# Kernel optimization log

Measured on AMD Instinct MI355X. Metric: run time of the kernel, lower is better.

The kernel has to match this reference:

```python
import jax, jax.numpy as jnp
import numpy as np
import math

B, S = 1, 2048
HID = 2048
H = 16
Q_LORA = 1536
KV_LORA = 512
ROPE_D = 64
NOPE_D = 128
V_D = 128
Q_HD = NOPE_D + ROPE_D  # 192
THETA = 10000.0
EPS = 1e-6


def rmsnorm(x, w):
    xf = x.astype(jnp.float32)
    n = xf * jax.lax.rsqrt(jnp.mean(xf * xf, axis=-1, keepdims=True) + EPS)
    return n.astype(x.dtype) * w


def rotate_half(x):
    d = x.shape[-1] // 2
    return jnp.concatenate([-x[..., d:], x[..., :d]], axis=-1)


def setup_inputs() -> dict:
    key = jax.random.key(0)
    ks = jax.random.split(key, 8)
    std = 0.02
    x = jax.random.normal(ks[0], (B, S, HID), dtype=jnp.float32)
    position = jnp.broadcast_to(jnp.arange(S, dtype=jnp.int32), (B, S))
    mask = jnp.broadcast_to(jnp.tril(jnp.ones((S, S), dtype=jnp.int32)), (B, S, S))
    Wq_down = jax.random.normal(ks[1], (HID, Q_LORA), dtype=jnp.float32) * std
    q_norm_w = jnp.ones((Q_LORA,), dtype=jnp.float32)
    Wq_up = jax.random.normal(ks[2], (Q_LORA, H * Q_HD), dtype=jnp.float32) * std
    Wkv_down = jax.random.normal(ks[3], (HID, KV_LORA + ROPE_D), dtype=jnp.float32) * std
    kv_norm_w = jnp.ones((KV_LORA,), dtype=jnp.float32)
    Wkv_up = jax.random.normal(ks[4], (KV_LORA, H * (NOPE_D + V_D)), dtype=jnp.float32) * std
    Wout = jax.random.normal(ks[5], (HID, HID), dtype=jnp.float32) * std
    return {"x": x, "position": position, "mask": mask,
            "Wq_down": Wq_down, "q_norm_w": q_norm_w, "Wq_up": Wq_up,
            "Wkv_down": Wkv_down, "kv_norm_w": kv_norm_w, "Wkv_up": Wkv_up,
            "Wout": Wout}


def reference(x, position, mask, Wq_down, q_norm_w, Wq_up, Wkv_down, kv_norm_w, Wkv_up, Wout):
    b, s, _ = x.shape
    # --- Q path: low-rank down -> RMSNorm -> up ---
    q = rmsnorm(x @ Wq_down, q_norm_w) @ Wq_up            # [B,S,H*Q_HD]
    q = q.reshape(b, s, H, Q_HD).transpose(0, 2, 1, 3)    # [B,H,S,Q_HD]
    q_nope, q_rope = q[..., :NOPE_D], q[..., NOPE_D:]
    # --- KV path ---
    c = x @ Wkv_down                                       # [B,S,KV_LORA+ROPE_D]
    c_kv, k_rope = c[..., :KV_LORA], c[..., KV_LORA:]
    kv = rmsnorm(c_kv, kv_norm_w) @ Wkv_up                 # [B,S,H*(NOPE_D+V_D)]
    kv = kv.reshape(b, s, H, NOPE_D + V_D).transpose(0, 2, 1, 3)
    k_nope, v_state = kv[..., :NOPE_D], kv[..., NOPE_D:]
    k_rope = k_rope[:, None]                               # [B,1,S,ROPE_D]
    # --- RoPE (decoupled, on rope dims only) ---
    inv_freq = 1.0 / (THETA ** (jnp.arange(0, ROPE_D, 2, dtype=jnp.float32) / ROPE_D))
    t = jnp.arange(s, dtype=jnp.float32)
    freqs = jnp.outer(t, inv_freq)                         # [S,ROPE_D/2]
    emb = jnp.concatenate([freqs, freqs], axis=-1)         # [S,ROPE_D]
    cos = jnp.cos(emb)[position][:, None]                  # [B,1,S,ROPE_D]
    sin = jnp.sin(emb)[position][:, None]
    q_rope = q_rope * cos + rotate_half(q_rope) * sin      # [B,H,S,ROPE_D]
    k_rope = k_rope * cos + rotate_half(k_rope) * sin      # [B,1,S,ROPE_D]
    k_rope = jnp.broadcast_to(k_rope, (b, H, s, ROPE_D))
    q_state = jnp.concatenate([q_nope, q_rope], axis=-1)   # [B,H,S,Q_HD]
    k_state = jnp.concatenate([k_nope, k_rope], axis=-1)   # [B,H,S,Q_HD]
    # --- attention (note: original scales by sqrt(v_head_dim)) ---
    scores = jnp.einsum('bhqd,bhkd->bhqk', q_state, k_state) / math.sqrt(V_D)
    scores = jnp.where(mask[:, None] == 0, -jnp.inf, scores)
    att_w = jax.nn.softmax(scores, axis=-1)
    att = jnp.einsum('bhqk,bhkd->bhqd', att_w, v_state)    # [B,H,S,V_D]
    att = att.transpose(0, 2, 1, 3).reshape(b, s, H * V_D) # [B,S,HID]
    return att @ Wout
```

## Files before the change

kernel.cpp:

```cpp
#include <hip/hip_runtime.h>
#include <hip/hip_bf16.h>
#include <math.h>

typedef __bf16 bf16_t;
typedef __bf16 bf16x4 __attribute__((ext_vector_type(4)));
typedef __bf16 bf16x8 __attribute__((ext_vector_type(8)));
typedef float f32x4 __attribute__((ext_vector_type(4)));

#define LOG2E 1.4426950408889634f

typedef const __attribute__((address_space(1))) void* as1cv;
typedef __attribute__((address_space(3))) void* as3v;

__device__ __forceinline__ void gload16(const bf16_t* g, bf16_t* l) {
  __builtin_amdgcn_global_load_lds((as1cv)g, (as3v)l, 16, 0, 0);
}

__global__ __launch_bounds__(256)
void prep_k(const float* __restrict__ x, const float* __restrict__ Wqd,
            const float* __restrict__ Wkvd, const float* __restrict__ Wqu,
            const float* __restrict__ Wkvu, const float* __restrict__ Wout,
            bf16_t* __restrict__ xb, bf16_t* __restrict__ WdT,
            bf16_t* __restrict__ WquT, bf16_t* __restrict__ WkvuT,
            bf16_t* __restrict__ WoutT) {
  __shared__ float t[32][33];
  const int tid = threadIdx.x;
  int bid = blockIdx.x;
  if (bid < 4096) {
    int i = (bid * 256 + tid) * 4;
    float4 v = *(const float4*)(x + i);
    bf16x4 o;
    o[0] = (bf16_t)v.x; o[1] = (bf16_t)v.y; o[2] = (bf16_t)v.z; o[3] = (bf16_t)v.w;
    *(bf16x4*)(xb + i) = o;
    return;
  }
  bid -= 4096;
  const float* in; bf16_t* out; int C, R, bx, by;
  if (bid < 3072)       { in = Wqd;  out = WdT;           R = 2048; C = 1536; bx = bid % 48;  by = bid / 48; }
  else if (bid < 4224)  { int b = bid - 3072;  in = Wkvd; out = WdT + 3145728; R = 2048; C = 576;  bx = b % 18;  by = b / 18; }
  else if (bid < 8832)  { int b = bid - 4224;  in = Wqu;  out = WquT;  R = 1536; C = 3072; bx = b % 96;  by = b / 96; }
  else if (bid < 10880) { int b = bid - 8832;  in = Wkvu; out = WkvuT; R = 512;  C = 4096; bx = b % 128; by = b / 128; }
  else                  { int b = bid - 10880; in = Wout; out = WoutT; R = 2048; C = 2048; bx = b % 64;  by = b / 64; }
  const int c0 = bx * 32, r0 = by * 32;
  const int tx = tid & 31, ty = tid >> 5;
#pragma unroll
  for (int i = 0; i < 32; i += 8)
    t[ty + i][tx] = in[(size_t)(r0 + ty + i) * C + c0 + tx];
  __syncthreads();
#pragma unroll
  for (int i = 0; i < 32; i += 8)
    out[(size_t)(c0 + ty + i) * R + r0 + tx] = (bf16_t)t[tx][ty + i];
}


__device__ __forceinline__ void stage8(const bf16_t* __restrict__ A,
                                       const bf16_t* __restrict__ Bt,
                                       int K, int N, int m0, int n0, int k0,
                                       bf16_t* As, bf16_t* Bs,
                                       int wave, int srow, int scol) {
#pragma unroll
  for (int i = 0; i < 2; ++i) {
    int r0 = (wave * 2 + i) * 8;
    gload16(A + (size_t)(m0 + r0 + srow) * K + k0 + scol, As + r0 * 64);
    int br = n0 + r0 + srow;
    if (br >= N) br = N - 1;
    gload16(Bt + (size_t)br * K + k0 + scol, Bs + r0 * 64);
  }
}

__device__ __forceinline__ void compute8(const bf16_t* As, const bf16_t* Bs,
                                         f32x4 (&acc)[2][4],
                                         int lane, int wr, int wc) {
  const int lm = lane & 15;
  const int sw = lm & 7;
#pragma unroll
  for (int ks = 0; ks < 2; ++ks) {
    const int ck = ((lane >> 4) + ks * 4) ^ sw;
    bf16x8 af[2], bfr[4];
#pragma unroll
    for (int i = 0; i < 2; ++i)
      af[i] = *(const bf16x8*)(As + (wr + i * 16 + lm) * 64 + ck * 8);
#pragma unroll
    for (int i = 0; i < 4; ++i)
      bfr[i] = *(const bf16x8*)(Bs + (wc + i * 16 + lm) * 64 + ck * 8);
#pragma unroll
    for (int mi = 0; mi < 2; ++mi)
#pragma unroll
      for (int ni = 0; ni < 4; ++ni)
        acc[mi][ni] = __builtin_amdgcn_mfma_f32_16x16x32_bf16(
            af[mi], bfr[ni], acc[mi][ni], 0, 0, 0);
  }
}

#define VMCNT(n) asm volatile("s_waitcnt vmcnt(" #n ")" ::: "memory")

__device__ __forceinline__ void gemm128_dbuf8(const bf16_t* __restrict__ A,
                                              const bf16_t* __restrict__ Bt,
                                              int K, int N, int m0, int n0,
                                              bf16_t* lds, f32x4 (&acc)[2][4],
                                              int wave, int lane) {
  const int srow = lane >> 3;
  const int scol = ((lane & 7) ^ srow) * 8;
  const int wr = (wave >> 1) * 32, wc = (wave & 1) * 64;
  bf16_t* A0 = lds;
  bf16_t* B0 = lds + 8192;
  bf16_t* A1 = lds + 16384;
  bf16_t* B1 = lds + 24576;
  const int nk = K >> 6;
  stage8(A, Bt, K, N, m0, n0, 0, A0, B0, wave, srow, scol);
  stage8(A, Bt, K, N, m0, n0, 64, A1, B1, wave, srow, scol);
  VMCNT(4);
  __builtin_amdgcn_s_barrier();
#pragma unroll 1
  for (int t = 0; t < nk; t += 2) {
    compute8(A0, B0, acc, lane, wr, wc);
    __builtin_amdgcn_s_barrier();
    if (t + 2 < nk) {
      stage8(A, Bt, K, N, m0, n0, (t + 2) << 6, A0, B0, wave, srow, scol);
      VMCNT(4);
    } else {
      VMCNT(0);
    }
    __builtin_amdgcn_s_barrier();
    compute8(A1, B1, acc, lane, wr, wc);
    if (t + 3 <= nk) {
      __builtin_amdgcn_s_barrier();
      if (t + 3 < nk) {
        stage8(A, Bt, K, N, m0, n0, (t + 3) << 6, A1, B1, wave, srow, scol);
        VMCNT(4);
      } else {
        VMCNT(0);
      }
      __builtin_amdgcn_s_barrier();
    }
  }
}

__global__ __launch_bounds__(512)
void gemm_dn8(const bf16_t* __restrict__ A, const bf16_t* __restrict__ Bt,
              bf16_t* __restrict__ C, int M, int N, int K) {
  __shared__ __align__(16) bf16_t lds[32768];
  const int tid = threadIdx.x;
  const int wave = tid >> 6, lane = tid & 63;
  const int m0 = blockIdx.y * 128, n0 = blockIdx.x * 128;
  const int wr = (wave >> 1) * 32, wc = (wave & 1) * 64;
  f32x4 acc[2][4] = {};
  gemm128_dbuf8(A, Bt, K, N, m0, n0, lds, acc, wave, lane);
  const int lm = lane & 15, lr = (lane >> 4) * 4;
#pragma unroll
  for (int mi = 0; mi < 2; ++mi)
#pragma unroll
    for (int ni = 0; ni < 4; ++ni) {
      int col = n0 + wc + ni * 16 + lm;
      if (col < N) {
#pragma unroll
        for (int i = 0; i < 4; ++i) {
          int row = m0 + wr + mi * 16 + lr + i;
          C[(size_t)row * N + col] = (bf16_t)acc[mi][ni][i];
        }
      }
    }
}

__global__ __launch_bounds__(512)
void gemm_outf8(const bf16_t* __restrict__ A, const bf16_t* __restrict__ Bt,
                float* __restrict__ C, int M, int N, int K) {
  __shared__ __align__(16) bf16_t lds[32768];
  const int tid = threadIdx.x;
  const int wave = tid >> 6, lane = tid & 63;
  const int m0 = blockIdx.y * 128, n0 = blockIdx.x * 128;
  const int wr = (wave >> 1) * 32, wc = (wave & 1) * 64;
  f32x4 acc[2][4] = {};
  gemm128_dbuf8(A, Bt, K, N, m0, n0, lds, acc, wave, lane);
  const int lm = lane & 15, lr = (lane >> 4) * 4;
#pragma unroll
  for (int mi = 0; mi < 2; ++mi)
#pragma unroll
    for (int ni = 0; ni < 4; ++ni) {
      int col = n0 + wc + ni * 16 + lm;
#pragma unroll
      for (int i = 0; i < 4; ++i) {
        int row = m0 + wr + mi * 16 + lr + i;
        C[(size_t)row * N + col] = acc[mi][ni][i];
      }
    }
}

__global__ __launch_bounds__(512)
void gemm_qkvup8(const bf16_t* __restrict__ qdn, const bf16_t* __restrict__ WquT,
                 const bf16_t* __restrict__ ckvn, const bf16_t* __restrict__ WkvuT,
                 const int* __restrict__ pos, bf16_t* __restrict__ qs,
                 bf16_t* __restrict__ ks, bf16_t* __restrict__ vt) {
  __shared__ __align__(16) bf16_t lds[32768];
  const int tid = threadIdx.x;
  const int wave = tid >> 6, lane = tid & 63;
  const int m0 = blockIdx.y * 128;
  const int wr = (wave >> 1) * 32, wc = (wave & 1) * 64;
  const int lm = lane & 15, lr = (lane >> 4) * 4;
  f32x4 acc[2][4] = {};
  if (blockIdx.x < 24) {
    const int n0 = blockIdx.x * 128;
    gemm128_dbuf8(qdn, WquT, 1536, 3072, m0, n0, lds, acc, wave, lane);
    const bool rope = (((n0 + wc) / 64) % 3) == 2;
    if (rope) {
#pragma unroll
      for (int mi = 0; mi < 2; ++mi)
#pragma unroll
        for (int i = 0; i < 4; ++i) {
          int row = m0 + wr + mi * 16 + lr + i;
          float p = (float)pos[row];
#pragma unroll
          for (int nl = 0; nl < 2; ++nl) {
            int fi = nl * 16 + lm;
            float ang = p * exp2f(-(float)fi * 0.41524101186092030f);
            float sn, cs;
            sincosf(ang, &sn, &cs);
            float v0 = acc[mi][nl][i], v1 = acc[mi][nl + 2][i];
            int c = n0 + wc + nl * 16 + lm;
            int h = c / 192, d = c - h * 192;
            bf16_t* base = qs + ((size_t)h * 2048 + row) * 192;
            base[d]      = (bf16_t)(v0 * cs - v1 * sn);
            base[d + 32] = (bf16_t)(v1 * cs + v0 * sn);
          }
        }
    } else {
#pragma unroll
      for (int mi = 0; mi < 2; ++mi)
#pragma unroll
        for (int ni = 0; ni < 4; ++ni) {
          int c = n0 + wc + ni * 16 + lm;
          int h = c / 192, d = c - h * 192;
#pragma unroll
          for (int i = 0; i < 4; ++i) {
            int row = m0 + wr + mi * 16 + lr + i;
            qs[((size_t)h * 2048 + row) * 192 + d] = (bf16_t)acc[mi][ni][i];
          }
        }
    }
  } else {
    const int n0 = (blockIdx.x - 24) * 128;
    gemm128_dbuf8(ckvn, WkvuT, 512, 4096, m0, n0, lds, acc, wave, lane);
#pragma unroll
    for (int mi = 0; mi < 2; ++mi)
#pragma unroll
      for (int ni = 0; ni < 4; ++ni) {
        int c = n0 + wc + ni * 16 + lm;
        int h = c >> 8, j = c & 255;
#pragma unroll
        for (int i = 0; i < 4; ++i) {
          int row = m0 + wr + mi * 16 + lr + i;
          bf16_t v = (bf16_t)acc[mi][ni][i];
          if (j < 128)
            ks[((size_t)h * 2048 + row) * 192 + j] = v;
          else
            vt[((size_t)h * 128 + (j - 128)) * 2048 + row] = v;
        }
      }
  }
}

__global__ __launch_bounds__(256)
void normrope_k(const bf16_t* __restrict__ Cd, const float* __restrict__ qnw,
                const float* __restrict__ kvnw, const int* __restrict__ pos,
                bf16_t* __restrict__ qdn, bf16_t* __restrict__ ckvn,
                bf16_t* __restrict__ ks) {
  __shared__ float red[4];
  const int bid = blockIdx.x, tid = threadIdx.x;
  if (bid < 4096) {
    const bf16_t* xr;
    const float* W;
    bf16_t* yr;
    int C;
    if (bid < 2048) {
      xr = Cd + (size_t)bid * 2112; W = qnw; yr = qdn + (size_t)bid * 1536; C = 1536;
    } else {
      int r = bid - 2048;
      xr = Cd + (size_t)r * 2112 + 1536; W = kvnw; yr = ckvn + (size_t)r * 512; C = 512;
    }
    int nch = C >> 3;
    bool act = tid < nch;
    float xv[8];
    float ss = 0.f;
    if (act) {
      bf16x8 v = *(const bf16x8*)(xr + tid * 8);
#pragma unroll
      for (int i = 0; i < 8; ++i) { xv[i] = (float)v[i]; ss += xv[i] * xv[i]; }
    }
#pragma unroll
    for (int off = 1; off < 64; off <<= 1) ss += __shfl_xor(ss, off, 64);
    if ((tid & 63) == 0) red[tid >> 6] = ss;
    __syncthreads();
    float tot = red[0] + red[1] + red[2] + red[3];
    float rs = rsqrtf(tot / (float)C + 1e-6f);
    if (act) {
      bf16x8 o;
#pragma unroll
      for (int i = 0; i < 8; ++i) {
        bf16_t nb = (bf16_t)(xv[i] * rs);
        o[i] = (bf16_t)((float)nb * W[tid * 8 + i]);
      }
      *(bf16x8*)(yr + tid * 8) = o;
    }
  } else {
    int s = bid - 4096, d = tid;
    if (d < 64) {
      float v = (float)Cd[(size_t)s * 2112 + 2048 + d];
      int fi = d & 31;
      float p = (float)pos[s];
      float ang = p * exp2f(-(float)fi * 0.415241011860920295f);
      float sn = sinf(ang), co = cosf(ang);
      float other = (float)Cd[(size_t)s * 2112 + 2048 + (d < 32 ? d + 32 : d - 32)];
      v = (d < 32) ? v * co - other * sn : v * co + other * sn;
      bf16_t bv = (bf16_t)v;
#pragma unroll
      for (int h = 0; h < 16; ++h)
        ks[((size_t)h * 2048 + s) * 192 + 128 + d] = bv;
    }
  }
}

__global__ __launch_bounds__(256)
void attn3_k(const bf16_t* __restrict__ Q, const bf16_t* __restrict__ Kst,
             const bf16_t* __restrict__ Vt, bf16_t* __restrict__ O,
             float* __restrict__ pbuf) {
  __shared__ __align__(16) bf16_t Ks[64 * 192];
  __shared__ __align__(16) bf16_t Vs[144 * 64];
  __shared__ __align__(16) bf16_t Ps[4][16 * 72];
  const int bid = blockIdx.x + (blockIdx.y << 8);
  const int lo = bid & 255;
  const int h = lo >> 4;
  const int jj = lo & 15;
  int t, kbeg, kend, sp = 0, pidx = 0;
  bool direct = false;
  if (bid < 256)      { t = 16 + jj; kbeg = 0;  kend = 16;    sp = 0; pidx = jj; }
  else if (bid < 512) { t = jj;      kbeg = 0;  kend = t + 1; direct = true; }
  else                { t = 31 - jj; kbeg = 16; kend = t + 1; sp = 1; pidx = 15 - jj; }
  const int q0 = t * 64;
  const int tid = threadIdx.x, wave = tid >> 6, lane = tid & 63;
  const int lm = lane & 15, lg = lane >> 4;
  const bf16_t* Qh = Q + (size_t)h * 2048 * 192;
  const bf16_t* Kh = Kst + (size_t)h * 2048 * 192;
  const bf16_t* Vh = Vt + (size_t)h * 128 * 2048;
  const float sc = 0.08838834764831845f * LOG2E;

  bf16x8 aq[6];
#pragma unroll
  for (int tt = 0; tt < 6; ++tt)
    aq[tt] = *(const bf16x8*)(Qh + (size_t)(q0 + wave * 16 + lm) * 192 + tt * 32 + lg * 8);

#pragma unroll
  for (int w = 0; w < 4; ++w) {
    int idx = w * 256 + tid;
    Vs[128 * 64 + idx] = (bf16_t)(idx < 64 ? 1.0f : 0.0f);
  }

  int kr[6], kc8[6], vr[4], vc8[4];
#pragma unroll
  for (int w = 0; w < 6; ++w) {
    int s = (wave * 6 + w) * 64 + lane;
    kr[w] = s / 24;
    kc8[w] = ((s % 24) ^ (kr[w] & 7)) * 8;
  }
#pragma unroll
  for (int w = 0; w < 4; ++w) {
    int s = (wave * 4 + w) * 64 + lane;
    vr[w] = s >> 3;
    vc8[w] = ((s & 7) ^ (vr[w] & 7)) * 8;
  }

  bf16x8 kstg[6], vstg[4];
  const int kb0 = kbeg * 64;
#pragma unroll
  for (int w = 0; w < 6; ++w)
    kstg[w] = *(const bf16x8*)(Kh + (size_t)(kb0 + kr[w]) * 192 + kc8[w]);
#pragma unroll
  for (int w = 0; w < 4; ++w)
    vstg[w] = *(const bf16x8*)(Vh + (size_t)vr[w] * 2048 + kb0 + vc8[w]);

  f32x4 o[9] = {};

  for (int kt = kbeg; kt < kend; ++kt) {
    const int k0 = kt * 64;
    if (kt != kbeg) __syncthreads();
#pragma unroll
    for (int w = 0; w < 6; ++w)
      *(bf16x8*)(Ks + ((wave * 6 + w) * 64 + lane) * 8) = kstg[w];
#pragma unroll
    for (int w = 0; w < 4; ++w)
      *(bf16x8*)(Vs + ((wave * 4 + w) * 64 + lane) * 8) = vstg[w];
    __syncthreads();

    if (kt + 1 < kend) {
      const int k1 = k0 + 64;
#pragma unroll
      for (int w = 0; w < 6; ++w)
        kstg[w] = *(const bf16x8*)(Kh + (size_t)(k1 + kr[w]) * 192 + kc8[w]);
#pragma unroll
      for (int w = 0; w < 4; ++w)
        vstg[w] = *(const bf16x8*)(Vh + (size_t)vr[w] * 2048 + k1 + vc8[w]);
    }

    f32x4 sa[4] = {};
    __builtin_amdgcn_s_setprio(1);
#pragma unroll
    for (int ct = 0; ct < 4; ++ct) {
#pragma unroll
      for (int tt = 0; tt < 6; ++tt) {
        int cc = (tt * 4 + lg) ^ (lm & 7);
        bf16x8 bk = *(const bf16x8*)(Ks + (ct * 16 + lm) * 192 + cc * 8);
        sa[ct] = __builtin_amdgcn_mfma_f32_16x16x32_bf16(aq[tt], bk, sa[ct], 0, 0, 0);
      }
    }
    __builtin_amdgcn_s_setprio(0);

    bf16_t* Pw = Ps[wave];
    const bool diag = (kt == t);
#pragma unroll
    for (int i = 0; i < 4; ++i) {
      const int row = q0 + wave * 16 + lg * 4 + i;
#pragma unroll
      for (int ct = 0; ct < 4; ++ct) {
        float p = exp2f(sa[ct][i] * sc);
        if (diag && (k0 + ct * 16 + lm > row)) p = 0.f;
        Pw[(lg * 4 + i) * 72 + ct * 16 + lm] = (bf16_t)p;
      }
    }
    __builtin_amdgcn_s_waitcnt(0xC07F);

    __builtin_amdgcn_s_setprio(1);
#pragma unroll
    for (int ks2 = 0; ks2 < 2; ++ks2) {
      bf16x8 ap = *(const bf16x8*)(Pw + lm * 72 + ks2 * 32 + lg * 8);
#pragma unroll
      for (int nt = 0; nt < 9; ++nt) {
        int rowv = nt * 16 + lm;
        int cc = (ks2 * 4 + lg) ^ (lm & 7);
        bf16x8 bv = *(const bf16x8*)(Vs + rowv * 64 + cc * 8);
        o[nt] = __builtin_amdgcn_mfma_f32_16x16x32_bf16(ap, bv, o[nt], 0, 0, 0);
      }
    }
    __builtin_amdgcn_s_setprio(0);
  }

  if (direct) {
#pragma unroll
    for (int i = 0; i < 4; ++i) {
      float l = __shfl(o[8][i], (lane & 48), 64);
      float inv = 1.f / l;
      int row = q0 + wave * 16 + lg * 4 + i;
#pragma unroll
      for (int nt = 0; nt < 8; ++nt)
        O[(size_t)row * 2048 + h * 128 + nt * 16 + lm] = (bf16_t)(o[nt][i] * inv);
    }
  } else {
    float* P = pbuf + ((size_t)(h * 16 + pidx) * 2 + sp) * 8448;
#pragma unroll
    for (int i = 0; i < 4; ++i) {
      int r = wave * 16 + lg * 4 + i;
#pragma unroll
      for (int nt = 0; nt < 8; ++nt)
        P[r * 132 + nt * 16 + lm] = o[nt][i];
      if (lm == 0) P[r * 132 + 128] = o[8][i];
    }
  }
}

__global__ __launch_bounds__(256)
void combine_k(const float* __restrict__ pbuf, bf16_t* __restrict__ O) {
  const int b = blockIdx.x, tid = threadIdx.x;
  const int h = b >> 4, pidx = b & 15;
  const int r = tid >> 2, c0 = (tid & 3) * 32;
  const float* p0 = pbuf + ((size_t)(h * 16 + pidx) * 2) * 8448 + r * 132;
  const float* p1 = p0 + 8448;
  const float inv = 1.f / (p0[128] + p1[128]);
  const int row = (16 + pidx) * 64 + r;
  bf16_t* dst = O + (size_t)row * 2048 + h * 128 + c0;
#pragma unroll
  for (int i = 0; i < 32; i += 4) {
    float4 a = *(const float4*)(p0 + c0 + i);
    float4 c = *(const float4*)(p1 + c0 + i);
    bf16x4 v;
    v[0] = (bf16_t)((a.x + c.x) * inv);
    v[1] = (bf16_t)((a.y + c.y) * inv);
    v[2] = (bf16_t)((a.z + c.z) * inv);
    v[3] = (bf16_t)((a.w + c.w) * inv);
    *(bf16x4*)(dst + i) = v;
  }
}

extern "C" void kernel_launch(void* const* d_in, const int* in_sizes, int n_in,
                              void* d_out, int out_size, void* d_ws, size_t ws_size,
                              hipStream_t stream) {
  const float* x    = (const float*)d_in[0];
  const int*   pos  = (const int*)d_in[1];
  const float* Wqd  = (const float*)d_in[3];
  const float* qnw  = (const float*)d_in[4];
  const float* Wqu  = (const float*)d_in[5];
  const float* Wkvd = (const float*)d_in[6];
  const float* kvnw = (const float*)d_in[7];
  const float* Wkvu = (const float*)d_in[8];
  const float* Wout = (const float*)d_in[9];
  float* out = (float*)d_out;

  bf16_t* arena = (bf16_t*)d_ws;
  bf16_t* xb    = arena;
  bf16_t* attb  = arena;
  bf16_t* WdT   = arena + 4194304;
  bf16_t* qdn   = arena + 4194304;
  bf16_t* WquT  = arena + 8519680;
  bf16_t* WkvuT = arena + 13238272;
  float*  pbuf  = (float*)(arena + 4194304);
  bf16_t* WoutT = arena + 15335424;
  bf16_t* Cdown = arena + 19529728;
  bf16_t* vt    = arena + 19529728;
  bf16_t* qs    = arena + 23855104;
  bf16_t* ks    = arena + 30146560;
  bf16_t* ckvn  = arena + 36438016;

  prep_k<<<dim3(19072), 256, 0, stream>>>(x, Wqd, Wkvd, Wqu, Wkvu, Wout,
                                          xb, WdT, WquT, WkvuT, WoutT);

  gemm_dn8<<<dim3(17, 16), 512, 0, stream>>>(xb, WdT, Cdown, 2048, 2112, 2048);

  normrope_k<<<dim3(6144), 256, 0, stream>>>(Cdown, qnw, kvnw, pos, qdn, ckvn, ks);

  gemm_qkvup8<<<dim3(56, 16), 512, 0, stream>>>(qdn, WquT, ckvn, WkvuT, pos,
                                                qs, ks, vt);

  attn3_k<<<dim3(256, 3), 256, 0, stream>>>(qs, ks, vt, attb, pbuf);

  combine_k<<<dim3(256), 256, 0, stream>>>(pbuf, attb);

  gemm_outf8<<<dim3(16, 16), 512, 0, stream>>>(attb, WoutT, out, 2048, 2048, 2048);
}
```

Measured before the change: 310.6 us.

## Double attention query tile to 128 rows per block, reusing K/V tiles

Each wave now handles two 16-row query groups, so every block covers 128 query rows and each K/V tile loaded into shared memory feeds twice as many MFMAs. The split-K work assignment and the partial-result buffer are remapped to 128-row tiles, which halves the grid to 384 blocks, and the combine kernel is resized to match. The aim is to cut K/V global and LDS traffic per unit of work. In exchange, register pressure rises (two sets of accumulators), the grid has fewer blocks, and causal masking is coarser.

```diff
diff --git a/kernel.cpp b/kernel.cpp
--- a/kernel.cpp
+++ b/kernel.cpp
@@ -319,23 +319,28 @@
   }
 }
 
-__global__ __launch_bounds__(256)
+__global__ __launch_bounds__(256, 2)
 void attn3_k(const bf16_t* __restrict__ Q, const bf16_t* __restrict__ Kst,
              const bf16_t* __restrict__ Vt, bf16_t* __restrict__ O,
              float* __restrict__ pbuf) {
   __shared__ __align__(16) bf16_t Ks[64 * 192];
   __shared__ __align__(16) bf16_t Vs[144 * 64];
-  __shared__ __align__(16) bf16_t Ps[4][16 * 72];
-  const int bid = blockIdx.x + (blockIdx.y << 8);
-  const int lo = bid & 255;
-  const int h = lo >> 4;
-  const int jj = lo & 15;
-  int t, kbeg, kend, sp = 0, pidx = 0;
+  __shared__ __align__(16) bf16_t Ps[4][32 * 72];
+  const int bid = blockIdx.x;
+  int h, T, kbeg, kend, sp = 1;
   bool direct = false;
-  if (bid < 256)      { t = 16 + jj; kbeg = 0;  kend = 16;    sp = 0; pidx = jj; }
-  else if (bid < 512) { t = jj;      kbeg = 0;  kend = t + 1; direct = true; }
-  else                { t = 31 - jj; kbeg = 16; kend = t + 1; sp = 1; pidx = 15 - jj; }
-  const int q0 = t * 64;
+  if (bid < 128) {
+    h = bid >> 3; int u = bid & 7; int up = u >> 1;
+    if ((u & 1) == 0) { T = 7 - up;  kbeg = 0;  kend = 2 * T + 2; direct = true; }
+    else              { T = 15 - up; kbeg = 16; kend = 2 * T + 2; }
+  } else if (bid < 256) {
+    h = (bid - 128) >> 3; T = 8 + ((bid - 128) & 7); kbeg = 0; kend = 16; sp = 0;
+  } else {
+    h = (bid - 256) >> 3; int u = (bid - 256) & 7; int up = u >> 1;
+    if ((u & 1) == 0) { T = up;     kbeg = 0;  kend = 2 * T + 2; direct = true; }
+    else              { T = 8 + up; kbeg = 16; kend = 2 * T + 2; }
+  }
+  const int q0 = T * 128;
   const int tid = threadIdx.x, wave = tid >> 6, lane = tid & 63;
   const int lm = lane & 15, lg = lane >> 4;
   const bf16_t* Qh = Q + (size_t)h * 2048 * 192;
@@ -343,10 +348,13 @@
   const bf16_t* Vh = Vt + (size_t)h * 128 * 2048;
   const float sc = 0.08838834764831845f * LOG2E;
 
-  bf16x8 aq[6];
-#pragma unroll
-  for (int tt = 0; tt < 6; ++tt)
-    aq[tt] = *(const bf16x8*)(Qh + (size_t)(q0 + wave * 16 + lm) * 192 + tt * 32 + lg * 8);
+  bf16x8 aq[2][6];
+#pragma unroll
+  for (int g = 0; g < 2; ++g)
+#pragma unroll
+    for (int tt = 0; tt < 6; ++tt)
+      aq[g][tt] = *(const bf16x8*)(Qh +
+          (size_t)(q0 + wave * 32 + g * 16 + lm) * 192 + tt * 32 + lg * 8);
 
 #pragma unroll
   for (int w = 0; w < 4; ++w) {
@@ -377,7 +385,7 @@
   for (int w = 0; w < 4; ++w)
     vstg[w] = *(const bf16x8*)(Vh + (size_t)vr[w] * 2048 + kb0 + vc8[w]);
 
-  f32x4 o[9] = {};
+  f32x4 o[2][9] = {};
 
   for (int kt = kbeg; kt < kend; ++kt) {
     const int k0 = kt * 64;
@@ -400,7 +408,7 @@
         vstg[w] = *(const bf16x8*)(Vh + (size_t)vr[w] * 2048 + k1 + vc8[w]);
     }
 
-    f32x4 sa[4] = {};
+    f32x4 sa[2][4] = {};
     __builtin_amdgcn_s_setprio(1);
 #pragma unroll
     for (int ct = 0; ct < 4; ++ct) {
@@ -408,35 +416,40 @@
       for (int tt = 0; tt < 6; ++tt) {
         int cc = (tt * 4 + lg) ^ (lm & 7);
         bf16x8 bk = *(const bf16x8*)(Ks + (ct * 16 + lm) * 192 + cc * 8);
-        sa[ct] = __builtin_amdgcn_mfma_f32_16x16x32_bf16(aq[tt], bk, sa[ct], 0, 0, 0);
+        sa[0][ct] = __builtin_amdgcn_mfma_f32_16x16x32_bf16(aq[0][tt], bk, sa[0][ct], 0, 0, 0);
+        sa[1][ct] = __builtin_amdgcn_mfma_f32_16x16x32_bf16(aq[1][tt], bk, sa[1][ct], 0, 0, 0);
       }
     }
     __builtin_amdgcn_s_setprio(0);
 
     bf16_t* Pw = Ps[wave];
-    const bool diag = (kt == t);
-#pragma unroll
-    for (int i = 0; i < 4; ++i) {
-      const int row = q0 + wave * 16 + lg * 4 + i;
-#pragma unroll
-      for (int ct = 0; ct < 4; ++ct) {
-        float p = exp2f(sa[ct][i] * sc);
-        if (diag && (k0 + ct * 16 + lm > row)) p = 0.f;
-        Pw[(lg * 4 + i) * 72 + ct * 16 + lm] = (bf16_t)p;
-      }
-    }
+    const bool diag = (kt >= 2 * T);
+#pragma unroll
+    for (int g = 0; g < 2; ++g)
+#pragma unroll
+      for (int i = 0; i < 4; ++i) {
+        const int row = q0 + wave * 32 + g * 16 + lg * 4 + i;
+#pragma unroll
+        for (int ct = 0; ct < 4; ++ct) {
+          float p = exp2f(sa[g][ct][i] * sc);
+          if (diag && (k0 + ct * 16 + lm > row)) p = 0.f;
+          Pw[(g * 16 + lg * 4 + i) * 72 + ct * 16 + lm] = (bf16_t)p;
+        }
+      }
     __builtin_amdgcn_s_waitcnt(0xC07F);
 
     __builtin_amdgcn_s_setprio(1);
 #pragma unroll
     for (int ks2 = 0; ks2 < 2; ++ks2) {
-      bf16x8 ap = *(const bf16x8*)(Pw + lm * 72 + ks2 * 32 + lg * 8);
+      bf16x8 ap0 = *(const bf16x8*)(Pw + lm * 72 + ks2 * 32 + lg * 8);
+      bf16x8 ap1 = *(const bf16x8*)(Pw + (16 + lm) * 72 + ks2 * 32 + lg * 8);
 #pragma unroll
       for (int nt = 0; nt < 9; ++nt) {
         int rowv = nt * 16 + lm;
         int cc = (ks2 * 4 + lg) ^ (lm & 7);
         bf16x8 bv = *(const bf16x8*)(Vs + rowv * 64 + cc * 8);
-        o[nt] = __builtin_amdgcn_mfma_f32_16x16x32_bf16(ap, bv, o[nt], 0, 0, 0);
+        o[0][nt] = __builtin_amdgcn_mfma_f32_16x16x32_bf16(ap0, bv, o[0][nt], 0, 0, 0);
+        o[1][nt] = __builtin_amdgcn_mfma_f32_16x16x32_bf16(ap1, bv, o[1][nt], 0, 0, 0);
       }
     }
     __builtin_amdgcn_s_setprio(0);
@@ -444,39 +457,43 @@
 
   if (direct) {
 #pragma unroll
-    for (int i = 0; i < 4; ++i) {
-      float l = __shfl(o[8][i], (lane & 48), 64);
-      float inv = 1.f / l;
-      int row = q0 + wave * 16 + lg * 4 + i;
-#pragma unroll
-      for (int nt = 0; nt < 8; ++nt)
-        O[(size_t)row * 2048 + h * 128 + nt * 16 + lm] = (bf16_t)(o[nt][i] * inv);
-    }
+    for (int g = 0; g < 2; ++g)
+#pragma unroll
+      for (int i = 0; i < 4; ++i) {
+        float l = __shfl(o[g][8][i], (lane & 48), 64);
+        float inv = 1.f / l;
+        int row = q0 + wave * 32 + g * 16 + lg * 4 + i;
+#pragma unroll
+        for (int nt = 0; nt < 8; ++nt)
+          O[(size_t)row * 2048 + h * 128 + nt * 16 + lm] = (bf16_t)(o[g][nt][i] * inv);
+      }
   } else {
-    float* P = pbuf + ((size_t)(h * 16 + pidx) * 2 + sp) * 8448;
-#pragma unroll
-    for (int i = 0; i < 4; ++i) {
-      int r = wave * 16 + lg * 4 + i;
-#pragma unroll
-      for (int nt = 0; nt < 8; ++nt)
-        P[r * 132 + nt * 16 + lm] = o[nt][i];
-      if (lm == 0) P[r * 132 + 128] = o[8][i];
-    }
+    float* P = pbuf + ((size_t)(h * 8 + (T - 8)) * 2 + sp) * 16896;
+#pragma unroll
+    for (int g = 0; g < 2; ++g)
+#pragma unroll
+      for (int i = 0; i < 4; ++i) {
+        int r = wave * 32 + g * 16 + lg * 4 + i;
+#pragma unroll
+        for (int nt = 0; nt < 8; ++nt)
+          P[r * 132 + nt * 16 + lm] = o[g][nt][i];
+        if (lm == 0) P[r * 132 + 128] = o[g][8][i];
+      }
   }
 }
 
 __global__ __launch_bounds__(256)
 void combine_k(const float* __restrict__ pbuf, bf16_t* __restrict__ O) {
   const int b = blockIdx.x, tid = threadIdx.x;
-  const int h = b >> 4, pidx = b & 15;
-  const int r = tid >> 2, c0 = (tid & 3) * 32;
-  const float* p0 = pbuf + ((size_t)(h * 16 + pidx) * 2) * 8448 + r * 132;
-  const float* p1 = p0 + 8448;
+  const int h = b >> 3, tt = b & 7;
+  const int r = tid >> 1, c0 = (tid & 1) * 64;
+  const float* p0 = pbuf + ((size_t)(h * 8 + tt) * 2) * 16896 + r * 132;
+  const float* p1 = p0 + 16896;
   const float inv = 1.f / (p0[128] + p1[128]);
-  const int row = (16 + pidx) * 64 + r;
+  const int row = (8 + tt) * 128 + r;
   bf16_t* dst = O + (size_t)row * 2048 + h * 128 + c0;
 #pragma unroll
-  for (int i = 0; i < 32; i += 4) {
+  for (int i = 0; i < 64; i += 4) {
     float4 a = *(const float4*)(p0 + c0 + i);
     float4 c = *(const float4*)(p1 + c0 + i);
     bf16x4 v;
@@ -527,9 +544,9 @@
   gemm_qkvup8<<<dim3(56, 16), 512, 0, stream>>>(qdn, WquT, ckvn, WkvuT, pos,
                                                 qs, ks, vt);
 
-  attn3_k<<<dim3(256, 3), 256, 0, stream>>>(qs, ks, vt, attb, pbuf);
-
-  combine_k<<<dim3(256), 256, 0, stream>>>(pbuf, attb);
+  attn3_k<<<dim3(384), 256, 0, stream>>>(qs, ks, vt, attb, pbuf);
+
+  combine_k<<<dim3(128), 256, 0, stream>>>(pbuf, attb);
 
   gemm_outf8<<<dim3(16, 16), 512, 0, stream>>>(attb, WoutT, out, 2048, 2048, 2048);
 }
```

Result: slower. 317.7 us (+2.3%).
